# Performance work log

Measured on AMD Instinct MI355X. Metric: run time of the kernel, lower is better.

## Reference

```python
import jax, jax.numpy as jnp
import numpy as np

N_NODES = 50000
N_EDGES = 800000
IN_C, HID_C, OUT_C = 512, 256, 128


def setup_inputs() -> dict:
    key = jax.random.key(0)
    k1, k2, k3, k4, k5, k6 = jax.random.split(key, 6)
    x = jax.random.normal(k1, (N_NODES, IN_C), dtype=jnp.float32)
    edge_index = jax.random.randint(k2, (2, N_EDGES), 0, N_NODES, dtype=jnp.int64)
    # Glorot-ish init for linear weights, zero bias (PyG GCNConv default)
    W1 = jax.random.normal(k3, (IN_C, HID_C), dtype=jnp.float32) / np.sqrt(IN_C)
    b1 = jnp.zeros((HID_C,), dtype=jnp.float32)
    W2 = jax.random.normal(k4, (HID_C, OUT_C), dtype=jnp.float32) / np.sqrt(HID_C)
    b2 = jnp.zeros((OUT_C,), dtype=jnp.float32)
    return {"x": x, "edge_index": edge_index, "W1": W1, "b1": b1, "W2": W2, "b2": b2}


def _gcn_layer(h, src, dst, norm, W, b, n_nodes):
    # h: [N, Fin] -> [N, Fout];  out_i = sum_{j->i} norm_e * (h W)_j + b
    h = h @ W
    msg = h[src] * norm[:, None]            # [E+N, Fout]
    out = jax.ops.segment_sum(msg, dst, num_segments=n_nodes)
    return out + b


def reference(x, edge_index, W1, b1, W2, b2):
    n = x.shape[0]
    loops = jnp.arange(n, dtype=edge_index.dtype)
    src = jnp.concatenate([edge_index[0], loops])  # add self-loops
    dst = jnp.concatenate([edge_index[1], loops])
    # symmetric normalization D^{-1/2} (A+I) D^{-1/2}
    deg = jax.ops.segment_sum(jnp.ones_like(src, dtype=x.dtype), dst, num_segments=n)
    dinv = jax.lax.rsqrt(jnp.maximum(deg, 1.0))
    norm = dinv[src] * dinv[dst]

    h = _gcn_layer(x, src, dst, norm, W1, b1, n)
    h = jax.nn.relu(h)
    # dropout: identity in eval mode (training=False)
    out = _gcn_layer(h, src, dst, norm, W2, b2, n)
    return out
```

## Files before the change

kernel.cpp:

```cpp
#include <hip/hip_runtime.h>
#include <hip/hip_bf16.h>

#define N_NODES 50000
#define N_EDGES 800000
#define IN_C 512
#define HID_C 256
#define OUT_C 128
#define SCAN_BLOCKS 49

typedef short bf16x8 __attribute__((ext_vector_type(8)));
typedef float f32x4 __attribute__((ext_vector_type(4)));

__device__ __forceinline__ float bf2f(unsigned short u) {
    return __uint_as_float(((unsigned)u) << 16);
}
__device__ __forceinline__ unsigned short f2bf(float f) {
    __hip_bfloat16 h = __float2bfloat16(f);
    return *(unsigned short*)&h;
}

__global__ void zero_counts_kernel(int* __restrict__ counts) {
    int i = blockIdx.x * blockDim.x + threadIdx.x;
    if (i < N_NODES) counts[i] = 0;
}

__global__ void count_kernel(const int* __restrict__ ei, int* __restrict__ counts) {
    int e = blockIdx.x * blockDim.x + threadIdx.x;
    if (e < N_EDGES) atomicAdd(&counts[ei[N_EDGES + e]], 1);
}

__global__ __launch_bounds__(256) void scan_part_kernel(const int* __restrict__ counts,
                                                        int* __restrict__ excl,
                                                        int* __restrict__ bsums) {
    __shared__ int tsum[256];
    const int t = threadIdx.x;
    const int base = blockIdx.x * 1024 + t * 4;
    int v[4];
    int s = 0;
#pragma unroll
    for (int j = 0; j < 4; j++) {
        int idx = base + j;
        v[j] = (idx < N_NODES) ? counts[idx] : 0;
        s += v[j];
    }
    tsum[t] = s;
    __syncthreads();
    for (int off = 1; off < 256; off <<= 1) {
        int add = (t >= off) ? tsum[t - off] : 0;
        __syncthreads();
        tsum[t] += add;
        __syncthreads();
    }
    int run = tsum[t] - s;
#pragma unroll
    for (int j = 0; j < 4; j++) {
        int idx = base + j;
        if (idx < N_NODES) excl[idx] = run;
        run += v[j];
    }
    if (t == 255) bsums[blockIdx.x] = tsum[255];
}

__global__ void scan_sums_kernel(int* __restrict__ bsums) {
    if (threadIdx.x == 0) {
        int r = 0;
        for (int i = 0; i < SCAN_BLOCKS; i++) {
            int tmp = bsums[i];
            bsums[i] = r;
            r += tmp;
        }
    }
}

__global__ void add_dinv_kernel(int* __restrict__ offsets, const int* __restrict__ bsums,
                                int* __restrict__ woff, const int* __restrict__ counts,
                                float* __restrict__ dinv) {
    int i = blockIdx.x * blockDim.x + threadIdx.x;
    if (i < N_NODES) {
        int o = offsets[i] + bsums[i >> 10];
        offsets[i] = o;
        woff[i] = o;
        dinv[i] = rsqrtf(1.0f + (float)counts[i]);
    }
    if (i == 0) offsets[N_NODES] = N_EDGES;
}

__global__ void fill_kernel(const int* __restrict__ ei, int* __restrict__ woff,
                            const float* __restrict__ dinv,
                            int* __restrict__ sorted_src, float* __restrict__ sorted_w) {
    int e = blockIdx.x * blockDim.x + threadIdx.x;
    if (e < N_EDGES) {
        int s = ei[e];
        int d = ei[N_EDGES + e];
        int pos = atomicAdd(&woff[d], 1);
        sorted_src[pos] = s;
        sorted_w[pos] = dinv[s];
    }
}

__global__ __launch_bounds__(256) void cast_x_kernel(const float* __restrict__ x,
                                                     unsigned short* __restrict__ xb) {
    size_t i = ((size_t)blockIdx.x * 256 + threadIdx.x) * 4;
    float4 v = *(const float4*)&x[i];
    ushort4 o;
    o.x = f2bf(v.x); o.y = f2bf(v.y); o.z = f2bf(v.z); o.w = f2bf(v.w);
    *(ushort4*)&xb[i] = o;
}

__global__ __launch_bounds__(256) void tcast_kernel(const float* __restrict__ W,
                                                    unsigned short* __restrict__ WT,
                                                    int K, int N) {
    int idx = blockIdx.x * 256 + threadIdx.x;
    int n = idx / K, k = idx - n * K;
    WT[idx] = f2bf(W[(size_t)k * N + n]);
}

__global__ __launch_bounds__(256) void mfma_gemm_bt(const unsigned short* __restrict__ A,
                                                    const unsigned short* __restrict__ BT,
                                                    unsigned short* __restrict__ C,
                                                    int M, int N, int K) {
    __shared__ unsigned short As[128 * 32];
    __shared__ unsigned short Bs[128 * 32];

    const int tid = threadIdx.x;
    const int w = tid >> 6;
    const int ln = tid & 63;
    const int br = blockIdx.y * 128;
    const int bc = blockIdx.x * 128;

    const int quad = ln >> 4;
    const int l16 = ln & 15;
    const int wr = (w >> 1) * 64;
    const int wc = (w & 1) * 64;

    const int crow = ln >> 2;
    const int koff = (ln & 3) * 8;

    f32x4 acc[4][4];
#pragma unroll
    for (int mt = 0; mt < 4; mt++)
#pragma unroll
        for (int nt = 0; nt < 4; nt++) acc[mt][nt] = (f32x4){0.f, 0.f, 0.f, 0.f};

    for (int kk = 0; kk < K; kk += 32) {
#pragma unroll
        for (int t = 0; t < 2; t++) {
            int c = w + t * 4;
            int row = br + c * 16 + crow;
            row = row < M ? row : M - 1;
            const unsigned short* gp = A + (size_t)row * K + kk + koff;
            unsigned short* lp = As + c * 512 + ln * 8;
            __builtin_amdgcn_global_load_lds((const __attribute__((address_space(1))) void*)gp,
                                             (__attribute__((address_space(3))) void*)lp,
                                             16, 0, 0);
        }
#pragma unroll
        for (int t = 0; t < 2; t++) {
            int c = w + t * 4;
            int row = bc + c * 16 + crow;
            const unsigned short* gp = BT + (size_t)row * K + kk + koff;
            unsigned short* lp = Bs + c * 512 + ln * 8;
            __builtin_amdgcn_global_load_lds((const __attribute__((address_space(1))) void*)gp,
                                             (__attribute__((address_space(3))) void*)lp,
                                             16, 0, 0);
        }
        __syncthreads();

        bf16x8 af[4], bfr[4];
#pragma unroll
        for (int mt = 0; mt < 4; mt++)
            af[mt] = *(const bf16x8*)&As[(wr + mt * 16 + l16) * 32 + quad * 8];
#pragma unroll
        for (int nt = 0; nt < 4; nt++)
            bfr[nt] = *(const bf16x8*)&Bs[(wc + nt * 16 + l16) * 32 + quad * 8];
#pragma unroll
        for (int mt = 0; mt < 4; mt++)
#pragma unroll
            for (int nt = 0; nt < 4; nt++)
                acc[mt][nt] = __builtin_amdgcn_mfma_f32_16x16x32_bf16(af[mt], bfr[nt],
                                                                      acc[mt][nt], 0, 0, 0);
        __syncthreads();
    }

#pragma unroll
    for (int mt = 0; mt < 4; mt++) {
#pragma unroll
        for (int r = 0; r < 4; r++) {
            int gr = br + wr + mt * 16 + quad * 4 + r;
            if (gr < M) {
#pragma unroll
                for (int nt = 0; nt < 4; nt++) {
                    int gc = bc + wc + nt * 16 + l16;
                    C[(size_t)gr * N + gc] = f2bf(acc[mt][nt][r]);
                }
            }
        }
    }
}

template <int C, bool RELU, bool BF16_OUT>
__global__ __launch_bounds__(256) void gather_agg_kernel(const int* __restrict__ offsets,
                                                         const int* __restrict__ ssrc,
                                                         const float* __restrict__ sw,
                                                         const unsigned short* __restrict__ H,
                                                         const float* __restrict__ dinv,
                                                         const float* __restrict__ bias,
                                                         void* __restrict__ outv) {
    constexpr int V = C / 64;
    const int node = blockIdx.x * 4 + (threadIdx.x >> 6);
    const int ln = threadIdx.x & 63;
    if (node >= N_NODES) return;
    const int c0 = ln * V;
    const float di = dinv[node];

    float acc[V];
    {
        const unsigned short* p = H + (size_t)node * C + c0;
        if (V == 4) {
            ushort4 u = *(const ushort4*)p;
            acc[0] = di * di * bf2f(u.x) + bias[c0 + 0];
            acc[1] = di * di * bf2f(u.y) + bias[c0 + 1];
            acc[2] = di * di * bf2f(u.z) + bias[c0 + 2];
            acc[3] = di * di * bf2f(u.w) + bias[c0 + 3];
        } else {
            ushort2 u = *(const ushort2*)p;
            acc[0] = di * di * bf2f(u.x) + bias[c0 + 0];
            acc[1] = di * di * bf2f(u.y) + bias[c0 + 1];
        }
    }

    int k = offsets[node];
    const int k1 = offsets[node + 1];
    for (; k + 1 < k1; k += 2) {
        int s0 = ssrc[k], s1 = ssrc[k + 1];
        float w0 = di * sw[k], w1 = di * sw[k + 1];
        const unsigned short* p0 = H + (size_t)s0 * C + c0;
        const unsigned short* p1 = H + (size_t)s1 * C + c0;
        if (V == 4) {
            ushort4 u0 = *(const ushort4*)p0;
            ushort4 u1 = *(const ushort4*)p1;
            acc[0] += w0 * bf2f(u0.x) + w1 * bf2f(u1.x);
            acc[1] += w0 * bf2f(u0.y) + w1 * bf2f(u1.y);
            acc[2] += w0 * bf2f(u0.z) + w1 * bf2f(u1.z);
            acc[3] += w0 * bf2f(u0.w) + w1 * bf2f(u1.w);
        } else {
            ushort2 u0 = *(const ushort2*)p0;
            ushort2 u1 = *(const ushort2*)p1;
            acc[0] += w0 * bf2f(u0.x) + w1 * bf2f(u1.x);
            acc[1] += w0 * bf2f(u0.y) + w1 * bf2f(u1.y);
        }
    }
    if (k < k1) {
        int s0 = ssrc[k];
        float w0 = di * sw[k];
        const unsigned short* p0 = H + (size_t)s0 * C + c0;
        if (V == 4) {
            ushort4 u0 = *(const ushort4*)p0;
            acc[0] += w0 * bf2f(u0.x);
            acc[1] += w0 * bf2f(u0.y);
            acc[2] += w0 * bf2f(u0.z);
            acc[3] += w0 * bf2f(u0.w);
        } else {
            ushort2 u0 = *(const ushort2*)p0;
            acc[0] += w0 * bf2f(u0.x);
            acc[1] += w0 * bf2f(u0.y);
        }
    }

    if (RELU) {
#pragma unroll
        for (int j = 0; j < V; j++) acc[j] = fmaxf(acc[j], 0.0f);
    }
    if (BF16_OUT) {
        unsigned short* out = (unsigned short*)outv;
        if (V == 4) {
            ushort4 o;
            o.x = f2bf(acc[0]); o.y = f2bf(acc[1]); o.z = f2bf(acc[2]); o.w = f2bf(acc[3]);
            *(ushort4*)&out[(size_t)node * C + c0] = o;
        } else {
            ushort2 o;
            o.x = f2bf(acc[0]); o.y = f2bf(acc[1]);
            *(ushort2*)&out[(size_t)node * C + c0] = o;
        }
    } else {
        float* out = (float*)outv;
        if (V == 4) {
            *(float4*)&out[(size_t)node * C + c0] = make_float4(acc[0], acc[1], acc[2], acc[3]);
        } else {
            *(float2*)&out[(size_t)node * C + c0] = make_float2(acc[0], acc[1]);
        }
    }
}

extern "C" void kernel_launch(void* const* d_in, const int* in_sizes, int n_in,
                              void* d_out, int out_size, void* d_ws, size_t ws_size,
                              hipStream_t stream) {
    const float* x  = (const float*)d_in[0];
    const int*   ei = (const int*)d_in[1];
    const float* W1 = (const float*)d_in[2];
    const float* b1 = (const float*)d_in[3];
    const float* W2 = (const float*)d_in[4];
    const float* b2 = (const float*)d_in[5];
    float* out = (float*)d_out;

    int*   counts     = (int*)d_ws;
    int*   offsets    = counts + 50048;
    int*   woff       = offsets + 50052;
    int*   bsums      = woff + 50048;
    float* dinv       = (float*)(bsums + 64);
    int*   sorted_src = (int*)(dinv + 50048);
    float* sorted_w   = (float*)(sorted_src + 800000);
    unsigned short* W1T = (unsigned short*)(sorted_w + 800000);
    unsigned short* W2T = W1T + 131072;
    unsigned short* xb  = W2T + 32768;
    unsigned short* H1  = xb + (size_t)N_NODES * IN_C;
    unsigned short* A1b = xb;
    unsigned short* H2  = xb + (size_t)N_NODES * HID_C;

    zero_counts_kernel<<<(N_NODES + 255) / 256, 256, 0, stream>>>(counts);
    count_kernel<<<(N_EDGES + 255) / 256, 256, 0, stream>>>(ei, counts);
    scan_part_kernel<<<SCAN_BLOCKS, 256, 0, stream>>>(counts, offsets, bsums);
    scan_sums_kernel<<<1, 64, 0, stream>>>(bsums);
    add_dinv_kernel<<<(N_NODES + 255) / 256, 256, 0, stream>>>(offsets, bsums, woff, counts, dinv);
    fill_kernel<<<(N_EDGES + 255) / 256, 256, 0, stream>>>(ei, woff, dinv, sorted_src, sorted_w);

    cast_x_kernel<<<(N_NODES * IN_C) / 1024, 256, 0, stream>>>(x, xb);
    tcast_kernel<<<(IN_C * HID_C) / 256, 256, 0, stream>>>(W1, W1T, IN_C, HID_C);
    tcast_kernel<<<(HID_C * OUT_C) / 256, 256, 0, stream>>>(W2, W2T, HID_C, OUT_C);

    {
        dim3 grid(HID_C / 128, (N_NODES + 127) / 128);
        mfma_gemm_bt<<<grid, 256, 0, stream>>>(xb, W1T, H1, N_NODES, HID_C, IN_C);
    }
    gather_agg_kernel<HID_C, true, true><<<(N_NODES + 3) / 4, 256, 0, stream>>>(
        offsets, sorted_src, sorted_w, H1, dinv, b1, (void*)A1b);

    {
        dim3 grid(OUT_C / 128, (N_NODES + 127) / 128);
        mfma_gemm_bt<<<grid, 256, 0, stream>>>(A1b, W2T, H2, N_NODES, OUT_C, HID_C);
    }
    gather_agg_kernel<OUT_C, false, false><<<(N_NODES + 3) / 4, 256, 0, stream>>>(
        offsets, sorted_src, sorted_w, H2, dinv, b2, (void*)out);
}
```

Baseline: 449.0 us.

## Split edges across lane groups with 16-byte loads and shuffle reduction in gather

The gather-aggregate kernel now gives each lane 8 contiguous bf16 channels, loaded with 16-byte vector reads. Each wavefront is split into several lane groups, and each group handles a strided subset of a node's edges. The partial sums are then combined with xor-shuffles. This gives more independent memory requests in flight per node and wider loads, at the cost of a cross-lane reduction and idle lanes during the output write. The block-sum scan is also turned from a serial single-thread loop into a wavefront shuffle scan.

```diff
diff --git a/kernel.cpp b/kernel.cpp
--- a/kernel.cpp
+++ b/kernel.cpp
@@ -62,14 +62,15 @@
 }
 
 __global__ void scan_sums_kernel(int* __restrict__ bsums) {
-    if (threadIdx.x == 0) {
-        int r = 0;
-        for (int i = 0; i < SCAN_BLOCKS; i++) {
-            int tmp = bsums[i];
-            bsums[i] = r;
-            r += tmp;
-        }
-    }
+    int ln = threadIdx.x;
+    int v = (ln < SCAN_BLOCKS) ? bsums[ln] : 0;
+    for (int off = 1; off < 64; off <<= 1) {
+        int u = __shfl_up(v, off, 64);
+        if (ln >= off) v += u;
+    }
+    int excl = __shfl_up(v, 1, 64);
+    if (ln == 0) excl = 0;
+    if (ln < SCAN_BLOCKS) bsums[ln] = excl;
 }
 
 __global__ void add_dinv_kernel(int* __restrict__ offsets, const int* __restrict__ bsums,
@@ -206,88 +207,63 @@
                                                          const float* __restrict__ dinv,
                                                          const float* __restrict__ bias,
                                                          void* __restrict__ outv) {
-    constexpr int V = C / 64;
+    constexpr int G = C / 8;
+    constexpr int NG = 64 / G;
     const int node = blockIdx.x * 4 + (threadIdx.x >> 6);
+    if (node >= N_NODES) return;
     const int ln = threadIdx.x & 63;
-    if (node >= N_NODES) return;
-    const int c0 = ln * V;
+    const int g = ln / G;
+    const int l = ln % G;
+    const int c0 = l * 8;
     const float di = dinv[node];
 
-    float acc[V];
-    {
-        const unsigned short* p = H + (size_t)node * C + c0;
-        if (V == 4) {
-            ushort4 u = *(const ushort4*)p;
-            acc[0] = di * di * bf2f(u.x) + bias[c0 + 0];
-            acc[1] = di * di * bf2f(u.y) + bias[c0 + 1];
-            acc[2] = di * di * bf2f(u.z) + bias[c0 + 2];
-            acc[3] = di * di * bf2f(u.w) + bias[c0 + 3];
-        } else {
-            ushort2 u = *(const ushort2*)p;
-            acc[0] = di * di * bf2f(u.x) + bias[c0 + 0];
-            acc[1] = di * di * bf2f(u.y) + bias[c0 + 1];
-        }
-    }
-
-    int k = offsets[node];
+    float acc[8] = {};
+    if (g == 0) {
+        bf16x8 h = *(const bf16x8*)&H[(size_t)node * C + c0];
+#pragma unroll
+        for (int j = 0; j < 8; j++)
+            acc[j] = di * di * bf2f((unsigned short)h[j]) + bias[c0 + j];
+    }
+
+    int k = offsets[node] + g;
     const int k1 = offsets[node + 1];
-    for (; k + 1 < k1; k += 2) {
-        int s0 = ssrc[k], s1 = ssrc[k + 1];
-        float w0 = di * sw[k], w1 = di * sw[k + 1];
-        const unsigned short* p0 = H + (size_t)s0 * C + c0;
-        const unsigned short* p1 = H + (size_t)s1 * C + c0;
-        if (V == 4) {
-            ushort4 u0 = *(const ushort4*)p0;
-            ushort4 u1 = *(const ushort4*)p1;
-            acc[0] += w0 * bf2f(u0.x) + w1 * bf2f(u1.x);
-            acc[1] += w0 * bf2f(u0.y) + w1 * bf2f(u1.y);
-            acc[2] += w0 * bf2f(u0.z) + w1 * bf2f(u1.z);
-            acc[3] += w0 * bf2f(u0.w) + w1 * bf2f(u1.w);
-        } else {
-            ushort2 u0 = *(const ushort2*)p0;
-            ushort2 u1 = *(const ushort2*)p1;
-            acc[0] += w0 * bf2f(u0.x) + w1 * bf2f(u1.x);
-            acc[1] += w0 * bf2f(u0.y) + w1 * bf2f(u1.y);
-        }
+    for (; k + NG < k1; k += 2 * NG) {
+        int s0 = ssrc[k], s1 = ssrc[k + NG];
+        float w0 = di * sw[k], w1 = di * sw[k + NG];
+        bf16x8 h0 = *(const bf16x8*)&H[(size_t)s0 * C + c0];
+        bf16x8 h1 = *(const bf16x8*)&H[(size_t)s1 * C + c0];
+#pragma unroll
+        for (int j = 0; j < 8; j++)
+            acc[j] += w0 * bf2f((unsigned short)h0[j]) + w1 * bf2f((unsigned short)h1[j]);
     }
     if (k < k1) {
         int s0 = ssrc[k];
         float w0 = di * sw[k];
-        const unsigned short* p0 = H + (size_t)s0 * C + c0;
-        if (V == 4) {
-            ushort4 u0 = *(const ushort4*)p0;
-            acc[0] += w0 * bf2f(u0.x);
-            acc[1] += w0 * bf2f(u0.y);
-            acc[2] += w0 * bf2f(u0.z);
-            acc[3] += w0 * bf2f(u0.w);
+        bf16x8 h0 = *(const bf16x8*)&H[(size_t)s0 * C + c0];
+#pragma unroll
+        for (int j = 0; j < 8; j++) acc[j] += w0 * bf2f((unsigned short)h0[j]);
+    }
+
+#pragma unroll
+    for (int m = G; m < 64; m <<= 1) {
+#pragma unroll
+        for (int j = 0; j < 8; j++) acc[j] += __shfl_xor(acc[j], m, 64);
+    }
+
+    if (g == 0) {
+        if (RELU) {
+#pragma unroll
+            for (int j = 0; j < 8; j++) acc[j] = fmaxf(acc[j], 0.0f);
+        }
+        if (BF16_OUT) {
+            bf16x8 o;
+#pragma unroll
+            for (int j = 0; j < 8; j++) o[j] = (short)f2bf(acc[j]);
+            *(bf16x8*)&((unsigned short*)outv)[(size_t)node * C + c0] = o;
         } else {
-            ushort2 u0 = *(const ushort2*)p0;
-            acc[0] += w0 * bf2f(u0.x);
-            acc[1] += w0 * bf2f(u0.y);
-        }
-    }
-
-    if (RELU) {
-#pragma unroll
-        for (int j = 0; j < V; j++) acc[j] = fmaxf(acc[j], 0.0f);
-    }
-    if (BF16_OUT) {
-        unsigned short* out = (unsigned short*)outv;
-        if (V == 4) {
-            ushort4 o;
-            o.x = f2bf(acc[0]); o.y = f2bf(acc[1]); o.z = f2bf(acc[2]); o.w = f2bf(acc[3]);
-            *(ushort4*)&out[(size_t)node * C + c0] = o;
-        } else {
-            ushort2 o;
-            o.x = f2bf(acc[0]); o.y = f2bf(acc[1]);
-            *(ushort2*)&out[(size_t)node * C + c0] = o;
-        }
-    } else {
-        float* out = (float*)outv;
-        if (V == 4) {
+            float* out = (float*)outv;
             *(float4*)&out[(size_t)node * C + c0] = make_float4(acc[0], acc[1], acc[2], acc[3]);
-        } else {
-            *(float2*)&out[(size_t)node * C + c0] = make_float2(acc[0], acc[1]);
+            *(float4*)&out[(size_t)node * C + c0 + 4] = make_float4(acc[4], acc[5], acc[6], acc[7]);
         }
     }
 }
```

After: 428.7 us. -4.5%, faster.
